# Kernel optimization log

Measured on AMD Instinct MI355X. Metric: run time of the kernel, lower is better.

Reference implementation:

```python
import jax, jax.numpy as jnp
import numpy as np

N, E, H = 50000, 800000, 128
HQ = H // 4  # 32


def _mlp(x, w1, b1, w2, b2):
    return jax.nn.relu(x @ w1 + b1) @ w2 + b2


def setup_inputs() -> dict:
    key = jax.random.key(0)
    ks = jax.random.split(key, 16)

    def lin(k, fan_in, fan_out):
        lim = 1.0 / np.sqrt(fan_in)
        kw, kb = jax.random.split(k)
        w = jax.random.uniform(kw, (fan_in, fan_out), jnp.float32, -lim, lim)
        b = jax.random.uniform(kb, (fan_out,), jnp.float32, -lim, lim)
        return w, b

    x = jax.random.normal(ks[0], (N, H), jnp.float32)
    pos = jax.random.normal(ks[1], (N, 3), jnp.float32)
    edge_index = jax.random.randint(ks[2], (2, E), 0, N, jnp.int64)

    pw1, pb1 = lin(ks[3], 3, HQ)
    pw2, pb2 = lin(ks[4], HQ, HQ)
    mw1, mb1 = lin(ks[5], 2 * H + HQ, H)
    mw2, mb2 = lin(ks[6], H, H)
    uw1, ub1 = lin(ks[7], 2 * H, H)
    uw2, ub2 = lin(ks[8], H, H)

    return dict(x=x, pos=pos, edge_index=edge_index,
                pw1=pw1, pb1=pb1, pw2=pw2, pb2=pb2,
                mw1=mw1, mb1=mb1, mw2=mw2, mb2=mb2,
                uw1=uw1, ub1=ub1, uw2=uw2, ub2=ub2)


def reference(x, pos, edge_index,
              pw1, pb1, pw2, pb2,
              mw1, mb1, mw2, mb2,
              uw1, ub1, uw2, ub2):
    row, col = edge_index[0], edge_index[1]
    # position features from relative positions [E, 3] -> [E, H//4]
    pos_feat = _mlp(pos[row] - pos[col], pw1, pb1, pw2, pb2)
    # per-edge messages [E, 2H + H//4] -> [E, H]
    msg_in = jnp.concatenate([x[row], x[col], pos_feat], axis=-1)
    messages = _mlp(msg_in, mw1, mb1, mw2, mb2)
    # scatter-add messages into destination nodes (index_add on col)
    agg = jax.ops.segment_sum(messages, col, num_segments=x.shape[0])
    # node update [N, 2H] -> [N, H]
    return _mlp(jnp.concatenate([x, agg], axis=-1), uw1, ub1, uw2, ub2)
```

## Files before the change

kernel.cpp:

```cpp
#include <hip/hip_runtime.h>
#include <hip/hip_bf16.h>

#define NN 50000
#define NE 800000
#define HD 128
#define SCAN_CHUNK 1024
#define SCAN_BLOCKS ((NN + SCAN_CHUNK - 1) / SCAN_CHUNK)

typedef __attribute__((ext_vector_type(8))) short s16x8;
typedef __attribute__((ext_vector_type(4))) float f32x4;

static __device__ __forceinline__ unsigned short f2bf(float f) {
    unsigned int u = __float_as_uint(f);
    u = (u + 0x7FFFu + ((u >> 16) & 1u)) >> 16;
    return (unsigned short)u;
}
static __device__ __forceinline__ float bf2f(unsigned short h) {
    return __uint_as_float(((unsigned int)h) << 16);
}
static __device__ __forceinline__ unsigned int f2bf2(float lo, float hi) {
    __hip_bfloat162 h = __float22bfloat162_rn(make_float2(lo, hi));
    return *reinterpret_cast<unsigned int*>(&h);
}

#define WFENCE() do { asm volatile("s_waitcnt lgkmcnt(0)" ::: "memory"); \
                      __builtin_amdgcn_sched_barrier(0); } while (0)

__global__ void prep_kernel(const float* __restrict__ pw2, const float* __restrict__ pb2,
                            const float* __restrict__ mw1, const float* __restrict__ mb1,
                            float* __restrict__ Wpc, float* __restrict__ bc)
{
    int tid = threadIdx.x;
    for (int idx = tid; idx < 32 * 128; idx += 256) {
        int j = idx >> 7, k = idx & 127;
        float s = 0.f;
        #pragma unroll 8
        for (int i = 0; i < 32; ++i) s += pw2[j * 32 + i] * mw1[(256 + i) * 128 + k];
        Wpc[idx] = s;
    }
    if (tid < 128) {
        float s = mb1[tid];
        #pragma unroll 8
        for (int i = 0; i < 32; ++i) s += pb2[i] * mw1[(256 + i) * 128 + tid];
        bc[tid] = s;
    }
}

__global__ void prep2_kernel(const float* __restrict__ mw2, const float* __restrict__ mb2,
                             const float* __restrict__ uw1,
                             float* __restrict__ W3, float* __restrict__ b3)
{
    int idx = blockIdx.x * 256 + threadIdx.x;
    if (idx < 128 * 128) {
        int k = idx >> 7, j = idx & 127;
        float s = 0.f;
        #pragma unroll 4
        for (int c = 0; c < 128; ++c)
            s += mw2[k * 128 + c] * uw1[(128 + c) * 128 + j];
        W3[idx] = s;
    }
    if (blockIdx.x == 0 && threadIdx.x < 128) {
        int j = threadIdx.x;
        float s = 0.f;
        #pragma unroll 4
        for (int c = 0; c < 128; ++c)
            s += mb2[c] * uw1[(128 + c) * 128 + j];
        b3[j] = s;
    }
}

__global__ void hist_kernel(const int* __restrict__ ei, int* __restrict__ cnt)
{
    __shared__ int sIdx64;
    if (threadIdx.x == 0) {
        int z = 1;
        for (int k = 0; k < 16; ++k) if (ei[2 * k + 1] != 0) z = 0;
        sIdx64 = z;
    }
    __syncthreads();
    int g = blockIdx.x * 256 + threadIdx.x;
    if (g >= NE / 2) return;
    int e0 = g * 2;
    int c0, c1;
    if (sIdx64) { int4 q = *(const int4*)&ei[2 * NE + 2 * e0]; c0 = q.x; c1 = q.z; }
    else        { int2 q = *(const int2*)&ei[NE + e0];         c0 = q.x; c1 = q.y; }
    atomicAdd(&cnt[c0], 1);
    atomicAdd(&cnt[c1], 1);
}

__global__ void scan1_kernel(const int* __restrict__ cnt, int* __restrict__ cursor,
                             int* __restrict__ bsum)
{
    __shared__ int tot[256];
    int b = blockIdx.x, t = threadIdx.x;
    int i0 = b * SCAN_CHUNK + t * 4;
    int v[4];
    #pragma unroll
    for (int k = 0; k < 4; ++k) v[k] = (i0 + k < NN) ? cnt[i0 + k] : 0;
    tot[t] = v[0] + v[1] + v[2] + v[3];
    __syncthreads();
    if (t == 0) {
        int run = 0;
        for (int i = 0; i < 256; ++i) { int x = tot[i]; tot[i] = run; run += x; }
        bsum[b] = run;
    }
    __syncthreads();
    int p = tot[t];
    #pragma unroll
    for (int k = 0; k < 4; ++k) {
        if (i0 + k < NN) cursor[i0 + k] = p;
        p += v[k];
    }
}

__global__ void scan2_kernel(int* __restrict__ bsum)
{
    if (threadIdx.x == 0) {
        int run = 0;
        for (int i = 0; i < SCAN_BLOCKS; ++i) { int x = bsum[i]; bsum[i] = run; run += x; }
    }
}

__global__ void scan3_kernel(int* __restrict__ cursor, const int* __restrict__ bsum)
{
    int b = blockIdx.x, t = threadIdx.x;
    int carry = bsum[b];
    int i0 = b * SCAN_CHUNK + t * 4;
    #pragma unroll
    for (int k = 0; k < 4; ++k)
        if (i0 + k < NN) cursor[i0 + k] += carry;
}

__global__ void scatter_kernel(const int* __restrict__ ei,
                               int* __restrict__ cursor, int2* __restrict__ sRC)
{
    __shared__ int sIdx64;
    if (threadIdx.x == 0) {
        int z = 1;
        for (int k = 0; k < 16; ++k) if (ei[2 * k + 1] != 0) z = 0;
        sIdx64 = z;
    }
    __syncthreads();
    int g = blockIdx.x * 256 + threadIdx.x;
    if (g >= NE / 2) return;
    int e0 = g * 2;
    int r0, r1, c0, c1;
    if (sIdx64) {
        int4 qr = *(const int4*)&ei[2 * e0];           r0 = qr.x; r1 = qr.z;
        int4 qc = *(const int4*)&ei[2 * NE + 2 * e0];  c0 = qc.x; c1 = qc.z;
    } else {
        int2 qr = *(const int2*)&ei[e0];       r0 = qr.x; r1 = qr.y;
        int2 qc = *(const int2*)&ei[NE + e0];  c0 = qc.x; c1 = qc.y;
    }
    int p0 = atomicAdd(&cursor[c0], 1);
    sRC[p0] = make_int2(r0, c0);
    int p1 = atomicAdd(&cursor[c1], 1);
    sRC[p1] = make_int2(r1, c1);
}

__global__ __launch_bounds__(256, 2) void node_pre_kernel(
    const float* __restrict__ x, const float* __restrict__ mw1,
    const float* __restrict__ bcv,
    unsigned short* __restrict__ xa, unsigned short* __restrict__ xb)
{
    __shared__ __align__(16) unsigned short sB[256 * 136];
    __shared__ __align__(16) unsigned short sSt[4][16 * 64];

    int tid = threadIdx.x;
    for (int idx = tid; idx < 256 * 128; idx += 256) {
        int c = idx & 255, k = idx >> 8;
        float v = (c < 128) ? mw1[k * 128 + c] : mw1[(128 + k) * 128 + (c - 128)];
        sB[c * 136 + k] = f2bf(v);
    }
    __syncthreads();

    int lane = tid & 63, wv = tid >> 6;
    int r16 = lane & 15, g4 = lane >> 4;
    unsigned short* st = sSt[wv];
    float bcx[8];
    #pragma unroll
    for (int i = 0; i < 8; ++i) bcx[i] = bcv[i * 16 + r16];
    const int NT = NN / 16;

    for (int t = blockIdx.x * 4 + wv; t < NT; t += gridDim.x * 4) {
        int r0 = t * 16;
        int row = r0 + r16;
        s16x8 a[4];
        #pragma unroll
        for (int ks = 0; ks < 4; ++ks) {
            const float* p = &x[(size_t)row * HD + ks * 32 + g4 * 8];
            float4 v0 = *(const float4*)p;
            float4 v1 = *(const float4*)(p + 4);
            union { s16x8 v; unsigned int u[4]; } av;
            av.u[0] = f2bf2(v0.x, v0.y); av.u[1] = f2bf2(v0.z, v0.w);
            av.u[2] = f2bf2(v1.x, v1.y); av.u[3] = f2bf2(v1.z, v1.w);
            a[ks] = av.v;
        }
        #pragma unroll
        for (int grp = 0; grp < 4; ++grp) {
            #pragma unroll
            for (int tc2 = 0; tc2 < 4; ++tc2) {
                int tc = grp * 4 + tc2;
                int col = tc * 16 + r16;
                f32x4 acc = {0.f, 0.f, 0.f, 0.f};
                #pragma unroll
                for (int ks = 0; ks < 4; ++ks) {
                    s16x8 b = *(const s16x8*)&sB[col * 136 + ks * 32 + g4 * 8];
                    acc = __builtin_amdgcn_mfma_f32_16x16x32_bf16(a[ks], b, acc, 0, 0, 0);
                }
                float badd = (grp >= 2) ? bcx[(grp - 2) * 4 + tc2] : 0.f;
                #pragma unroll
                for (int j = 0; j < 4; ++j)
                    st[(g4 * 4 + j) * 64 + tc2 * 16 + r16] = f2bf(acc[j] + badd);
            }
            WFENCE();
            unsigned short* dst = (grp < 2) ? xa : xb;
            int ch = (grp & 1) * 64;
            #pragma unroll
            for (int i = 0; i < 2; ++i) {
                int idx = i * 512 + lane * 8;
                int rr = idx >> 6, cc = idx & 63;
                *(s16x8*)&dst[(size_t)(r0 + rr) * HD + ch + cc] = *(const s16x8*)&st[idx];
            }
            WFENCE();
        }
    }
}

__global__ __launch_bounds__(256, 3) void edge_kernel(
    const float* __restrict__ pos, const int2* __restrict__ sRC,
    const float* __restrict__ pw1, const float* __restrict__ pb1,
    const unsigned short* __restrict__ xa, const unsigned short* __restrict__ xb,
    const float* __restrict__ Wpc,
    float* __restrict__ aggH)
{
    __shared__ __align__(16) unsigned short sT[4][16 * 136];
    __shared__ int sECs[4][16];

    int tid = threadIdx.x;
    int lane = tid & 63, wv = tid >> 6;
    int r16 = lane & 15, g4 = lane >> 4;
    unsigned short* stg = sT[wv];
    int* secw = sECs[wv];

    s16x8 wr[8];
    #pragma unroll
    for (int tc = 0; tc < 8; ++tc) {
        s16x8 w;
        #pragma unroll
        for (int i = 0; i < 8; ++i)
            w[i] = (short)f2bf(Wpc[(g4 * 8 + i) * 128 + tc * 16 + r16]);
        wr[tc] = w;
    }
    float pw10[8], pw11[8], pw12[8], pb1r[8];
    #pragma unroll
    for (int i = 0; i < 8; ++i) {
        int k = g4 * 8 + i;
        pw10[i] = pw1[k]; pw11[i] = pw1[32 + k]; pw12[i] = pw1[64 + k];
        pb1r[i] = pb1[k];
    }

    const int NW = gridDim.x * 4;
    const int NT = NE / 16;
    int gw = blockIdx.x * 4 + wv;
    if (gw >= NT) return;

    int2 rc = sRC[gw * 16 + r16];
    int2 rcN = rc;
    if (gw + NW < NT) rcN = sRC[(gw + NW) * 16 + r16];
    float dp0 = pos[rc.x * 3 + 0] - pos[rc.y * 3 + 0];
    float dp1 = pos[rc.x * 3 + 1] - pos[rc.y * 3 + 1];
    float dp2 = pos[rc.x * 3 + 2] - pos[rc.y * 3 + 2];
    s16x8 ga[4], gb[4];
    #pragma unroll
    for (int s = 0; s < 4; ++s) {
        int gx = __shfl(rc.x, s * 4 + g4, 64);
        int gy = __shfl(rc.y, s * 4 + g4, 64);
        ga[s] = *(const s16x8*)&xa[(size_t)gx * HD + r16 * 8];
        gb[s] = *(const s16x8*)&xb[(size_t)gy * HD + r16 * 8];
    }

    for (int t = gw; t < NT; t += NW) {
        bool hn  = (t + NW) < NT;
        bool hn2 = (t + 2 * NW) < NT;

        #pragma unroll
        for (int s = 0; s < 4; ++s) {
            union { s16x8 v; unsigned int u[4]; } o;
            #pragma unroll
            for (int i2 = 0; i2 < 4; ++i2) {
                float v0 = bf2f((unsigned short)ga[s][2 * i2]) +
                           bf2f((unsigned short)gb[s][2 * i2]);
                float v1 = bf2f((unsigned short)ga[s][2 * i2 + 1]) +
                           bf2f((unsigned short)gb[s][2 * i2 + 1]);
                o.u[i2] = f2bf2(v0, v1);
            }
            *(s16x8*)&stg[(s * 4 + g4) * 136 + r16 * 8] = o.v;
        }
        if (lane < 16) secw[lane] = rc.y;
        WFENCE();

        if (hn) {
            #pragma unroll
            for (int s = 0; s < 4; ++s) {
                int gx = __shfl(rcN.x, s * 4 + g4, 64);
                int gy = __shfl(rcN.y, s * 4 + g4, 64);
                ga[s] = *(const s16x8*)&xa[(size_t)gx * HD + r16 * 8];
                gb[s] = *(const s16x8*)&xb[(size_t)gy * HD + r16 * 8];
            }
        }

        int2 rcN2 = rcN;
        if (hn2) rcN2 = sRC[(t + 2 * NW) * 16 + r16];

        float dp0N = 0.f, dp1N = 0.f, dp2N = 0.f;
        if (hn) {
            dp0N = pos[rcN.x * 3 + 0] - pos[rcN.y * 3 + 0];
            dp1N = pos[rcN.x * 3 + 1] - pos[rcN.y * 3 + 1];
            dp2N = pos[rcN.x * 3 + 2] - pos[rcN.y * 3 + 2];
        }

        union { s16x8 v; unsigned int u[4]; } apf;
        #pragma unroll
        for (int i2 = 0; i2 < 4; ++i2) {
            int i = 2 * i2;
            float v0 = fmaf(dp0, pw10[i], fmaf(dp1, pw11[i], fmaf(dp2, pw12[i], pb1r[i])));
            float v1 = fmaf(dp0, pw10[i+1], fmaf(dp1, pw11[i+1], fmaf(dp2, pw12[i+1], pb1r[i+1])));
            apf.u[i2] = f2bf2(fmaxf(v0, 0.f), fmaxf(v1, 0.f));
        }

        #pragma unroll
        for (int tc = 0; tc < 8; ++tc) {
            f32x4 acc;
            #pragma unroll
            for (int j = 0; j < 4; ++j)
                acc[j] = bf2f(stg[(g4 * 4 + j) * 136 + tc * 16 + r16]);
            acc = __builtin_amdgcn_mfma_f32_16x16x32_bf16(apf.v, wr[tc], acc, 0, 0, 0);
            #pragma unroll
            for (int j = 0; j < 4; ++j)
                stg[(g4 * 4 + j) * 136 + tc * 16 + r16] = f2bf(fmaxf(acc[j], 0.f));
        }
        WFENCE();

        {
            int f0 = lane, f1 = lane + 64;
            int cur = secw[0];
            float run0 = bf2f(stg[f0]);
            float run1 = bf2f(stg[f1]);
            #pragma unroll
            for (int e = 1; e < 16; ++e) {
                int c = secw[e];
                float v0 = bf2f(stg[e * 136 + f0]);
                float v1 = bf2f(stg[e * 136 + f1]);
                if (c != cur) {
                    unsafeAtomicAdd(&aggH[(size_t)cur * HD + f0], run0);
                    unsafeAtomicAdd(&aggH[(size_t)cur * HD + f1], run1);
                    cur = c; run0 = v0; run1 = v1;
                } else { run0 += v0; run1 += v1; }
            }
            unsafeAtomicAdd(&aggH[(size_t)cur * HD + f0], run0);
            unsafeAtomicAdd(&aggH[(size_t)cur * HD + f1], run1);
        }
        WFENCE();

        rc = rcN; rcN = rcN2; dp0 = dp0N; dp1 = dp1N; dp2 = dp2N;
    }
}

__global__ __launch_bounds__(512, 2) void upd_kernel(
    const float* __restrict__ x, const float* __restrict__ aggH,
    const int* __restrict__ cnt,
    const float* __restrict__ uw1, const float* __restrict__ ub1,
    const float* __restrict__ W3, const float* __restrict__ b3,
    const float* __restrict__ uw2, const float* __restrict__ ub2,
    float* __restrict__ out)
{
    __shared__ __align__(16) unsigned short sB1a[128 * 136];
    __shared__ __align__(16) unsigned short sW3l[128 * 136];
    __shared__ __align__(16) unsigned short sB2[128 * 136];
    __shared__ __align__(16) unsigned short sSt[8][16 * 136];

    int tid = threadIdx.x;
    for (int idx = tid; idx < 128 * 128; idx += 512) {
        int c = idx & 127, k = idx >> 7;
        sB1a[c * 136 + k] = f2bf(uw1[k * 128 + c]);
        sW3l[c * 136 + k] = f2bf(W3[k * 128 + c]);
        sB2[c * 136 + k]  = f2bf(uw2[k * 128 + c]);
    }
    __syncthreads();

    int lane = tid & 63, wv = tid >> 6;
    int r16 = lane & 15, g4 = lane >> 4;
    unsigned short* st = sSt[wv];
    float ub1r[8], ub2r[8], b3r[8];
    #pragma unroll
    for (int tc = 0; tc < 8; ++tc) {
        ub1r[tc] = ub1[tc * 16 + r16];
        ub2r[tc] = ub2[tc * 16 + r16];
        b3r[tc]  = b3[tc * 16 + r16];
    }

    const int NT = NN / 16;
    for (int t = blockIdx.x * 8 + wv; t < NT; t += gridDim.x * 8) {
        int r0 = t * 16;
        int row = r0 + r16;
        s16x8 a[8];
        #pragma unroll
        for (int ks = 0; ks < 8; ++ks) {
            const float* p = (ks < 4) ? &x[(size_t)row * HD + ks * 32 + g4 * 8]
                                      : &aggH[(size_t)row * HD + (ks - 4) * 32 + g4 * 8];
            float4 v0 = *(const float4*)p;
            float4 v1 = *(const float4*)(p + 4);
            union { s16x8 v; unsigned int u[4]; } av;
            av.u[0] = f2bf2(v0.x, v0.y); av.u[1] = f2bf2(v0.z, v0.w);
            av.u[2] = f2bf2(v1.x, v1.y); av.u[3] = f2bf2(v1.z, v1.w);
            a[ks] = av.v;
        }
        float cn[4];
        #pragma unroll
        for (int j = 0; j < 4; ++j) cn[j] = (float)cnt[r0 + g4 * 4 + j];

        #pragma unroll
        for (int tc = 0; tc < 8; ++tc) {
            int col = tc * 16 + r16;
            f32x4 acc;
            #pragma unroll
            for (int j = 0; j < 4; ++j) acc[j] = ub1r[tc] + cn[j] * b3r[tc];
            #pragma unroll
            for (int ks = 0; ks < 4; ++ks) {
                s16x8 b = *(const s16x8*)&sB1a[col * 136 + ks * 32 + g4 * 8];
                acc = __builtin_amdgcn_mfma_f32_16x16x32_bf16(a[ks], b, acc, 0, 0, 0);
            }
            #pragma unroll
            for (int ks = 4; ks < 8; ++ks) {
                s16x8 b = *(const s16x8*)&sW3l[col * 136 + (ks - 4) * 32 + g4 * 8];
                acc = __builtin_amdgcn_mfma_f32_16x16x32_bf16(a[ks], b, acc, 0, 0, 0);
            }
            #pragma unroll
            for (int j = 0; j < 4; ++j)
                st[(g4 * 4 + j) * 136 + col] = f2bf(fmaxf(acc[j], 0.f));
        }
        WFENCE();
        s16x8 a2[4];
        #pragma unroll
        for (int ks = 0; ks < 4; ++ks)
            a2[ks] = *(const s16x8*)&st[r16 * 136 + ks * 32 + g4 * 8];
        WFENCE();
        #pragma unroll
        for (int tc = 0; tc < 8; ++tc) {
            int col = tc * 16 + r16;
            float bv = ub2r[tc];
            f32x4 acc = {bv, bv, bv, bv};
            #pragma unroll
            for (int ks = 0; ks < 4; ++ks) {
                s16x8 b = *(const s16x8*)&sB2[col * 136 + ks * 32 + g4 * 8];
                acc = __builtin_amdgcn_mfma_f32_16x16x32_bf16(a2[ks], b, acc, 0, 0, 0);
            }
            #pragma unroll
            for (int j = 0; j < 4; ++j)
                out[(size_t)(r0 + g4 * 4 + j) * HD + col] = acc[j];
        }
    }
}

extern "C" void kernel_launch(void* const* d_in, const int* in_sizes, int n_in,
                              void* d_out, int out_size, void* d_ws, size_t ws_size,
                              hipStream_t stream)
{
    const float* x   = (const float*)d_in[0];
    const float* pos = (const float*)d_in[1];
    const int*   ei  = (const int*)d_in[2];
    const float* pw1 = (const float*)d_in[3];
    const float* pb1 = (const float*)d_in[4];
    const float* pw2 = (const float*)d_in[5];
    const float* pb2 = (const float*)d_in[6];
    const float* mw1 = (const float*)d_in[7];
    const float* mb1 = (const float*)d_in[8];
    const float* mw2 = (const float*)d_in[9];
    const float* mb2 = (const float*)d_in[10];
    const float* uw1 = (const float*)d_in[11];
    const float* ub1 = (const float*)d_in[12];
    const float* uw2 = (const float*)d_in[13];
    const float* ub2 = (const float*)d_in[14];
    float* out = (float*)d_out;

    char* ws = (char*)d_ws;
    float*          aggH   = (float*)(ws);
    unsigned short* xa     = (unsigned short*)(ws + 25600000);
    unsigned short* xb     = (unsigned short*)(ws + 38400000);
    float*          Wpc    = (float*)(ws + 51200000);
    float*          bcv    = (float*)(ws + 51216384);
    int*            cnt    = (int*)(ws + 51216896);
    int*            cursor = (int*)(ws + 51417600);
    int*            bsum   = (int*)(ws + 51618304);
    int2*           sRC    = (int2*)(ws + 51618560);

    float* W3 = (float*)(ws + 51417600);
    float* b3 = (float*)(ws + 51417600 + 65536);

    hipMemsetAsync(aggH, 0, (size_t)NN * HD * sizeof(float), stream);
    hipMemsetAsync(cnt, 0, NN * sizeof(int), stream);
    prep_kernel<<<1, 256, 0, stream>>>(pw2, pb2, mw1, mb1, Wpc, bcv);
    hist_kernel<<<(NE / 2 + 255) / 256, 256, 0, stream>>>(ei, cnt);
    scan1_kernel<<<SCAN_BLOCKS, 256, 0, stream>>>(cnt, cursor, bsum);
    scan2_kernel<<<1, 64, 0, stream>>>(bsum);
    scan3_kernel<<<SCAN_BLOCKS, 256, 0, stream>>>(cursor, bsum);
    scatter_kernel<<<(NE / 2 + 255) / 256, 256, 0, stream>>>(ei, cursor, sRC);
    prep2_kernel<<<64, 256, 0, stream>>>(mw2, mb2, uw1, W3, b3);
    node_pre_kernel<<<512, 256, 0, stream>>>(x, mw1, bcv, xa, xb);
    edge_kernel<<<1536, 256, 0, stream>>>(pos, sRC, pw1, pb1, xa, xb, Wpc, aggH);
    upd_kernel<<<256, 512, 0, stream>>>(x, aggH, cnt, uw1, ub1, W3, b3, uw2, ub2, out);
}
```

Before: 251.7 us.

## Permute node projection layout so edge kernel feeds MFMA accumulators from registers

Node projections xa/xb are now stored in a permuted column order, computed by two separate kernels. This lets the edge kernel add the gathered xa+xb values directly into the MFMA accumulator registers and drop a shared-memory staging round trip and one wave fence per tile. The segmented reduction reads through the matching permutation, and the edge grid is halved. The trade-offs are an extra launch that re-reads x, and different LDS access patterns that may cause bank conflicts.

```diff
diff --git a/kernel.cpp b/kernel.cpp
--- a/kernel.cpp
+++ b/kernel.cpp
@@ -158,28 +158,23 @@
     sRC[p1] = make_int2(r1, c1);
 }
 
-__global__ __launch_bounds__(256, 2) void node_pre_kernel(
+__global__ __launch_bounds__(256, 3) void node_a_kernel(
     const float* __restrict__ x, const float* __restrict__ mw1,
-    const float* __restrict__ bcv,
-    unsigned short* __restrict__ xa, unsigned short* __restrict__ xb)
-{
-    __shared__ __align__(16) unsigned short sB[256 * 136];
-    __shared__ __align__(16) unsigned short sSt[4][16 * 64];
+    unsigned short* __restrict__ xa)
+{
+    __shared__ __align__(16) unsigned short sB[128 * 136];
+    __shared__ __align__(16) unsigned short sSt[4][16 * 132];
 
     int tid = threadIdx.x;
-    for (int idx = tid; idx < 256 * 128; idx += 256) {
-        int c = idx & 255, k = idx >> 8;
-        float v = (c < 128) ? mw1[k * 128 + c] : mw1[(128 + k) * 128 + (c - 128)];
-        sB[c * 136 + k] = f2bf(v);
+    for (int idx = tid; idx < 128 * 128; idx += 256) {
+        int c = idx & 127, k = idx >> 7;
+        sB[c * 136 + k] = f2bf(mw1[k * 128 + c]);
     }
     __syncthreads();
 
     int lane = tid & 63, wv = tid >> 6;
     int r16 = lane & 15, g4 = lane >> 4;
     unsigned short* st = sSt[wv];
-    float bcx[8];
-    #pragma unroll
-    for (int i = 0; i < 8; ++i) bcx[i] = bcv[i * 16 + r16];
     const int NT = NN / 16;
 
     for (int t = blockIdx.x * 4 + wv; t < NT; t += gridDim.x * 4) {
@@ -196,34 +191,103 @@
             av.u[2] = f2bf2(v1.x, v1.y); av.u[3] = f2bf2(v1.z, v1.w);
             a[ks] = av.v;
         }
-        #pragma unroll
-        for (int grp = 0; grp < 4; ++grp) {
-            #pragma unroll
-            for (int tc2 = 0; tc2 < 4; ++tc2) {
-                int tc = grp * 4 + tc2;
-                int col = tc * 16 + r16;
-                f32x4 acc = {0.f, 0.f, 0.f, 0.f};
+        float hold[4];
+        #pragma unroll
+        for (int tc = 0; tc < 8; ++tc) {
+            int col = tc * 16 + r16;
+            f32x4 acc = {0.f, 0.f, 0.f, 0.f};
+            #pragma unroll
+            for (int ks = 0; ks < 4; ++ks) {
+                s16x8 b = *(const s16x8*)&sB[col * 136 + ks * 32 + g4 * 8];
+                acc = __builtin_amdgcn_mfma_f32_16x16x32_bf16(a[ks], b, acc, 0, 0, 0);
+            }
+            if ((tc & 1) == 0) {
                 #pragma unroll
-                for (int ks = 0; ks < 4; ++ks) {
-                    s16x8 b = *(const s16x8*)&sB[col * 136 + ks * 32 + g4 * 8];
-                    acc = __builtin_amdgcn_mfma_f32_16x16x32_bf16(a[ks], b, acc, 0, 0, 0);
-                }
-                float badd = (grp >= 2) ? bcx[(grp - 2) * 4 + tc2] : 0.f;
+                for (int j = 0; j < 4; ++j) hold[j] = acc[j];
+            } else {
                 #pragma unroll
                 for (int j = 0; j < 4; ++j)
-                    st[(g4 * 4 + j) * 64 + tc2 * 16 + r16] = f2bf(acc[j] + badd);
-            }
-            WFENCE();
-            unsigned short* dst = (grp < 2) ? xa : xb;
-            int ch = (grp & 1) * 64;
-            #pragma unroll
-            for (int i = 0; i < 2; ++i) {
-                int idx = i * 512 + lane * 8;
-                int rr = idx >> 6, cc = idx & 63;
-                *(s16x8*)&dst[(size_t)(r0 + rr) * HD + ch + cc] = *(const s16x8*)&st[idx];
-            }
-            WFENCE();
-        }
+                    *(unsigned int*)&st[(g4 * 4 + j) * 132 + r16 * 8 + (tc - 1)] =
+                        f2bf2(hold[j], acc[j]);
+            }
+        }
+        WFENCE();
+        #pragma unroll
+        for (int i = 0; i < 4; ++i) {
+            int idx = i * 512 + lane * 8;
+            int rr = idx >> 7, cc = idx & 127;
+            *(s16x8*)&xa[(size_t)(r0 + rr) * HD + cc] = *(const s16x8*)&st[rr * 132 + cc];
+        }
+        WFENCE();
+    }
+}
+
+__global__ __launch_bounds__(256, 3) void node_b_kernel(
+    const float* __restrict__ x, const float* __restrict__ mw1,
+    const float* __restrict__ bcv,
+    unsigned short* __restrict__ xb)
+{
+    __shared__ __align__(16) unsigned short sB[128 * 136];
+    __shared__ __align__(16) unsigned short sSt[4][16 * 132];
+
+    int tid = threadIdx.x;
+    for (int idx = tid; idx < 128 * 128; idx += 256) {
+        int c = idx & 127, k = idx >> 7;
+        sB[c * 136 + k] = f2bf(mw1[(128 + k) * 128 + c]);
+    }
+    __syncthreads();
+
+    int lane = tid & 63, wv = tid >> 6;
+    int r16 = lane & 15, g4 = lane >> 4;
+    unsigned short* st = sSt[wv];
+    float bcr[8];
+    #pragma unroll
+    for (int tc = 0; tc < 8; ++tc) bcr[tc] = bcv[tc * 16 + r16];
+    const int NT = NN / 16;
+
+    for (int t = blockIdx.x * 4 + wv; t < NT; t += gridDim.x * 4) {
+        int r0 = t * 16;
+        int row = r0 + r16;
+        s16x8 a[4];
+        #pragma unroll
+        for (int ks = 0; ks < 4; ++ks) {
+            const float* p = &x[(size_t)row * HD + ks * 32 + g4 * 8];
+            float4 v0 = *(const float4*)p;
+            float4 v1 = *(const float4*)(p + 4);
+            union { s16x8 v; unsigned int u[4]; } av;
+            av.u[0] = f2bf2(v0.x, v0.y); av.u[1] = f2bf2(v0.z, v0.w);
+            av.u[2] = f2bf2(v1.x, v1.y); av.u[3] = f2bf2(v1.z, v1.w);
+            a[ks] = av.v;
+        }
+        float hold[4];
+        #pragma unroll
+        for (int tc = 0; tc < 8; ++tc) {
+            int col = tc * 16 + r16;
+            float bv = bcr[tc];
+            f32x4 acc = {bv, bv, bv, bv};
+            #pragma unroll
+            for (int ks = 0; ks < 4; ++ks) {
+                s16x8 b = *(const s16x8*)&sB[col * 136 + ks * 32 + g4 * 8];
+                acc = __builtin_amdgcn_mfma_f32_16x16x32_bf16(a[ks], b, acc, 0, 0, 0);
+            }
+            if ((tc & 1) == 0) {
+                #pragma unroll
+                for (int j = 0; j < 4; ++j) hold[j] = acc[j];
+            } else {
+                #pragma unroll
+                for (int j = 0; j < 4; ++j)
+                    *(unsigned int*)&st[(g4 * 4 + j) * 132 + r16 * 8 + (tc - 1)] =
+                        f2bf2(hold[j], acc[j]);
+            }
+        }
+        WFENCE();
+        #pragma unroll
+        for (int i = 0; i < 4; ++i) {
+            int idx = i * 512 + lane * 8;
+            int rr = idx >> 7, cc = idx & 127;
+            *(s16x8*)&xb[(size_t)(r0 + rr) * HD + cc] = *(const s16x8*)&st[rr * 132 + cc];
+        }
+        WFENCE();
     }
 }
 
@@ -273,46 +337,59 @@
     float dp2 = pos[rc.x * 3 + 2] - pos[rc.y * 3 + 2];
     s16x8 ga[4], gb[4];
     #pragma unroll
-    for (int s = 0; s < 4; ++s) {
-        int gx = __shfl(rc.x, s * 4 + g4, 64);
-        int gy = __shfl(rc.y, s * 4 + g4, 64);
-        ga[s] = *(const s16x8*)&xa[(size_t)gx * HD + r16 * 8];
-        gb[s] = *(const s16x8*)&xb[(size_t)gy * HD + r16 * 8];
+    for (int j = 0; j < 4; ++j) {
+        int gx = __shfl(rc.x, g4 * 4 + j, 64);
+        int gy = __shfl(rc.y, g4 * 4 + j, 64);
+        ga[j] = *(const s16x8*)&xa[(size_t)gx * HD + r16 * 8];
+        gb[j] = *(const s16x8*)&xb[(size_t)gy * HD + r16 * 8];
     }
 
     for (int t = gw; t < NT; t += NW) {
         bool hn  = (t + NW) < NT;
         bool hn2 = (t + 2 * NW) < NT;
 
-        #pragma unroll
-        for (int s = 0; s < 4; ++s) {
-            union { s16x8 v; unsigned int u[4]; } o;
-            #pragma unroll
-            for (int i2 = 0; i2 < 4; ++i2) {
-                float v0 = bf2f((unsigned short)ga[s][2 * i2]) +
-                           bf2f((unsigned short)gb[s][2 * i2]);
-                float v1 = bf2f((unsigned short)ga[s][2 * i2 + 1]) +
-                           bf2f((unsigned short)gb[s][2 * i2 + 1]);
-                o.u[i2] = f2bf2(v0, v1);
-            }
-            *(s16x8*)&stg[(s * 4 + g4) * 136 + r16 * 8] = o.v;
-        }
         if (lane < 16) secw[lane] = rc.y;
+        union { s16x8 v; unsigned int u[4]; } apf;
+        #pragma unroll
+        for (int i2 = 0; i2 < 4; ++i2) {
+            int i = 2 * i2;
+            float v0 = fmaf(dp0, pw10[i], fmaf(dp1, pw11[i], fmaf(dp2, pw12[i], pb1r[i])));
+            float v1 = fmaf(dp0, pw10[i+1], fmaf(dp1, pw11[i+1], fmaf(dp2, pw12[i+1], pb1r[i+1])));
+            apf.u[i2] = f2bf2(fmaxf(v0, 0.f), fmaxf(v1, 0.f));
+        }
+
+        float hold[4];
+        #pragma unroll
+        for (int tc = 0; tc < 8; ++tc) {
+            f32x4 acc;
+            #pragma unroll
+            for (int j = 0; j < 4; ++j)
+                acc[j] = bf2f((unsigned short)ga[j][tc]) + bf2f((unsigned short)gb[j][tc]);
+            acc = __builtin_amdgcn_mfma_f32_16x16x32_bf16(apf.v, wr[tc], acc, 0, 0, 0);
+            if ((tc & 1) == 0) {
+                #pragma unroll
+                for (int j = 0; j < 4; ++j) hold[j] = fmaxf(acc[j], 0.f);
+            } else {
+                #pragma unroll
+                for (int j = 0; j < 4; ++j)
+                    *(unsigned int*)&stg[(g4 * 4 + j) * 136 + r16 * 8 + (tc - 1)] =
+                        f2bf2(hold[j], fmaxf(acc[j], 0.f));
+            }
+        }
         WFENCE();
 
         if (hn) {
             #pragma unroll
-            for (int s = 0; s < 4; ++s) {
-                int gx = __shfl(rcN.x, s * 4 + g4, 64);
-                int gy = __shfl(rcN.y, s * 4 + g4, 64);
-                ga[s] = *(const s16x8*)&xa[(size_t)gx * HD + r16 * 8];
-                gb[s] = *(const s16x8*)&xb[(size_t)gy * HD + r16 * 8];
+            for (int j = 0; j < 4; ++j) {
+                int gx = __shfl(rcN.x, g4 * 4 + j, 64);
+                int gy = __shfl(rcN.y, g4 * 4 + j, 64);
+                ga[j] = *(const s16x8*)&xa[(size_t)gx * HD + r16 * 8];
+                gb[j] = *(const s16x8*)&xb[(size_t)gy * HD + r16 * 8];
             }
         }
 
         int2 rcN2 = rcN;
         if (hn2) rcN2 = sRC[(t + 2 * NW) * 16 + r16];
-
         float dp0N = 0.f, dp1N = 0.f, dp2N = 0.f;
         if (hn) {
             dp0N = pos[rcN.x * 3 + 0] - pos[rcN.y * 3 + 0];
@@ -320,46 +397,25 @@
             dp2N = pos[rcN.x * 3 + 2] - pos[rcN.y * 3 + 2];
         }
 
-        union { s16x8 v; unsigned int u[4]; } apf;
-        #pragma unroll
-        for (int i2 = 0; i2 < 4; ++i2) {
-            int i = 2 * i2;
-            float v0 = fmaf(dp0, pw10[i], fmaf(dp1, pw11[i], fmaf(dp2, pw12[i], pb1r[i])));
-            float v1 = fmaf(dp0, pw10[i+1], fmaf(dp1, pw11[i+1], fmaf(dp2, pw12[i+1], pb1r[i+1])));
-            apf.u[i2] = f2bf2(fmaxf(v0, 0.f), fmaxf(v1, 0.f));
-        }
-
-        #pragma unroll
-        for (int tc = 0; tc < 8; ++tc) {
-            f32x4 acc;
-            #pragma unroll
-            for (int j = 0; j < 4; ++j)
-                acc[j] = bf2f(stg[(g4 * 4 + j) * 136 + tc * 16 + r16]);
-            acc = __builtin_amdgcn_mfma_f32_16x16x32_bf16(apf.v, wr[tc], acc, 0, 0, 0);
-            #pragma unroll
-            for (int j = 0; j < 4; ++j)
-                stg[(g4 * 4 + j) * 136 + tc * 16 + r16] = f2bf(fmaxf(acc[j], 0.f));
-        }
-        WFENCE();
-
         {
-            int f0 = lane, f1 = lane + 64;
+            int p0 = (lane & 15) * 8 + (lane >> 4);
+            int p1 = p0 + 4;
             int cur = secw[0];
-            float run0 = bf2f(stg[f0]);
-            float run1 = bf2f(stg[f1]);
+            float run0 = bf2f(stg[p0]);
+            float run1 = bf2f(stg[p1]);
             #pragma unroll
             for (int e = 1; e < 16; ++e) {
                 int c = secw[e];
-                float v0 = bf2f(stg[e * 136 + f0]);
-                float v1 = bf2f(stg[e * 136 + f1]);
+                float v0 = bf2f(stg[e * 136 + p0]);
+                float v1 = bf2f(stg[e * 136 + p1]);
                 if (c != cur) {
-                    unsafeAtomicAdd(&aggH[(size_t)cur * HD + f0], run0);
-                    unsafeAtomicAdd(&aggH[(size_t)cur * HD + f1], run1);
+                    unsafeAtomicAdd(&aggH[(size_t)cur * HD + lane], run0);
+                    unsafeAtomicAdd(&aggH[(size_t)cur * HD + lane + 64], run1);
                     cur = c; run0 = v0; run1 = v1;
                 } else { run0 += v0; run1 += v1; }
             }
-            unsafeAtomicAdd(&aggH[(size_t)cur * HD + f0], run0);
-            unsafeAtomicAdd(&aggH[(size_t)cur * HD + f1], run1);
+            unsafeAtomicAdd(&aggH[(size_t)cur * HD + lane], run0);
+            unsafeAtomicAdd(&aggH[(size_t)cur * HD + lane + 64], run1);
         }
         WFENCE();
 
@@ -507,7 +563,8 @@
     scan3_kernel<<<SCAN_BLOCKS, 256, 0, stream>>>(cursor, bsum);
     scatter_kernel<<<(NE / 2 + 255) / 256, 256, 0, stream>>>(ei, cursor, sRC);
     prep2_kernel<<<64, 256, 0, stream>>>(mw2, mb2, uw1, W3, b3);
-    node_pre_kernel<<<512, 256, 0, stream>>>(x, mw1, bcv, xa, xb);
-    edge_kernel<<<1536, 256, 0, stream>>>(pos, sRC, pw1, pb1, xa, xb, Wpc, aggH);
+    node_a_kernel<<<512, 256, 0, stream>>>(x, mw1, xa);
+    node_b_kernel<<<512, 256, 0, stream>>>(x, mw1, bcv, xb);
+    edge_kernel<<<768, 256, 0, stream>>>(pos, sRC, pw1, pb1, xa, xb, Wpc, aggH);
     upd_kernel<<<256, 512, 0, stream>>>(x, aggH, cnt, uw1, ub1, W3, b3, uw2, ub2, out);
 }
```

New measurement: 244.1 us. 1.03x faster.
